# Kernel tuning notes

Measured on AMD Instinct MI355X. Metric: run time of the kernel, lower is better.

## Reference

```python
import jax, jax.numpy as jnp
import numpy as np

N, E, D_IN, L, H, U = 20000, 320000, 256, 4, 4, 64
HID = H * U  # 256
OUT = 64
LN_EPS = 1e-3  # keras LayerNormalization default epsilon
NEG_SLOPE = 0.2


def layer_norm(x, g, b):
    m = jnp.mean(x, axis=-1, keepdims=True)
    v = jnp.var(x, axis=-1, keepdims=True)
    return (x - m) * jax.lax.rsqrt(v + LN_EPS) * g + b


def gatv2(x, dst, src, Wl, Wr, a):
    # x: [N, HID]; Wl/Wr: [HID, H, U]; a: [H, U]
    zl = jnp.einsum('nd,dhu->nhu', x, Wl)  # target projection
    zr = jnp.einsum('nd,dhu->nhu', x, Wr)  # source projection / messages
    f = jax.nn.leaky_relu(zl[dst] + zr[src], NEG_SLOPE)       # [E, H, U]
    s = jnp.einsum('ehu,hu->eh', f, a)                        # [E, H]
    smax = jax.ops.segment_max(s, dst, num_segments=N)        # [N, H]
    es = jnp.exp(s - smax[dst])
    denom = jax.ops.segment_sum(es, dst, num_segments=N)      # [N, H]
    agg = jax.ops.segment_sum(es[:, :, None] * zr[src], dst, num_segments=N)
    agg = agg / (denom[:, :, None] + 1e-9)                    # [N, H, U]
    return agg.reshape(N, HID) + x  # residual (input dim == H*U)


def setup_inputs() -> dict:
    key = jax.random.key(0)
    ks = jax.random.split(key, 10)
    s_in = 1.0 / np.sqrt(D_IN)
    s_h = 1.0 / np.sqrt(HID)
    return {
        'x': jax.random.normal(ks[0], (N, D_IN), jnp.float32),
        'head_W': jax.random.normal(ks[1], (D_IN, HID), jnp.float32) * s_in,
        'head_b': jnp.zeros((HID,), jnp.float32),
        'ng_g': jnp.ones((L, HID), jnp.float32),
        'ng_b': jnp.zeros((L, HID), jnp.float32),
        'Wl': jax.random.normal(ks[2], (L, HID, H, U), jnp.float32) * s_h,
        'Wr': jax.random.normal(ks[3], (L, HID, H, U), jnp.float32) * s_h,
        'att': jax.random.normal(ks[4], (L, H, U), jnp.float32) * (1.0 / np.sqrt(U)),
        'nd_g': jnp.ones((L, HID), jnp.float32),
        'nd_b': jnp.zeros((L, HID), jnp.float32),
        'dense_W': jax.random.normal(ks[5], (L, HID, 4 * HID), jnp.float32) * s_h,
        'dense_b': jnp.zeros((L, 4 * HID), jnp.float32),
        'tail_W': jax.random.normal(ks[6], (HID, OUT), jnp.float32) * s_h,
        'tail_b': jnp.zeros((OUT,), jnp.float32),
        'edges': jax.random.randint(ks[7], (E, 2), 0, N, jnp.int32),
    }


def reference(x, head_W, head_b, ng_g, ng_b, Wl, Wr, att, nd_g, nd_b,
              dense_W, dense_b, tail_W, tail_b, edges):
    dst, src = edges[:, 0], edges[:, 1]
    h = x @ head_W + head_b  # head_layer
    for l in range(L):
        h = layer_norm(h, ng_g[l], ng_b[l])
        h = gatv2(h, dst, src, Wl[l], Wr[l], att[l])
        xr = layer_norm(h, nd_g[l], nd_b[l])
        # inference: dropout is identity
        d = jax.nn.gelu(xr @ dense_W[l] + dense_b[l], approximate=True)  # [N, 4*HID]
        h = d.reshape(N, 4, HID).sum(axis=1) + xr  # Add(split(.,4)) + residual
    return h @ tail_W + tail_b
```

## Files before the change

kernel.cpp:

```cpp
#include <hip/hip_runtime.h>
#include <cstdint>

#define NN 20000
#define EE 320000
#define DHID 256

typedef short bf16x8 __attribute__((ext_vector_type(8)));
typedef float f32x4 __attribute__((ext_vector_type(4)));


__device__ __forceinline__ float b2f(unsigned short u) {
    union { unsigned int i; float f; } v;
    v.i = ((unsigned int)u) << 16;
    return v.f;
}

__device__ __forceinline__ void b2f2(unsigned int w, float& lo, float& hi) {
    union { unsigned int i; float f; } a, c;
    a.i = w << 16;
    c.i = w & 0xffff0000u;
    lo = a.f;
    hi = c.f;
}

__device__ __forceinline__ unsigned short f2b(float x) {
    union { float f; unsigned int i; } v;
    v.f = x;
    unsigned int r = (v.i + 0x7FFFu + ((v.i >> 16) & 1u)) >> 16;
    return (unsigned short)r;
}

__device__ __forceinline__ float wave_sum(float v) {
#pragma unroll
    for (int m = 1; m < 64; m <<= 1) v += __shfl_xor(v, m);
    return v;
}

#define DPP_ROR_ADD(v, n)                                                                  \
    v += __int_as_float(__builtin_amdgcn_update_dpp(__float_as_int(v), __float_as_int(v),  \
                                                    0x120 + (n), 0xF, 0xF, 0))
__device__ __forceinline__ float quad16_sum(float v) {
    DPP_ROR_ADD(v, 8);
    DPP_ROR_ADD(v, 4);
    DPP_ROR_ADD(v, 2);
    DPP_ROR_ADD(v, 1);
    return v;
}

__device__ __forceinline__ float gelu_f(float x) {
    float x2 = x * x;
    float p  = fmaf(0.044715f, x2, 1.0f);
    float e  = __expf(x * p * 1.5957691216f);
    float r  = 1.0f / (e + 1.0f);
    return x - x * r;
}

__device__ __forceinline__ void gld16(const unsigned short* g, unsigned short* lds) {
    __builtin_amdgcn_global_load_lds((const __attribute__((address_space(1))) unsigned int*)g,
                                     (__attribute__((address_space(3))) unsigned int*)lds, 16, 0, 0);
}


__global__ void hist_kernel(const int* __restrict__ edges, int* __restrict__ counts, int E_) {
    int e = blockIdx.x * 256 + threadIdx.x;
    if (e >= E_) return;
    atomicAdd(&counts[edges[e * 2]], 1);
}

__global__ void pad_counts(const int* __restrict__ counts, int* __restrict__ pc, int n) {
    int i = blockIdx.x * 256 + threadIdx.x;
    if (i < n) pc[i] = (counts[i] + 3) & ~3;
}

__global__ __launch_bounds__(1024) void scan_block(const int* __restrict__ counts,
                                                   int* __restrict__ excl,
                                                   int* __restrict__ bsums, int n) {
    __shared__ int sd[1024];
    int tid = threadIdx.x;
    int i = blockIdx.x * 1024 + tid;
    int c = (i < n) ? counts[i] : 0;
    sd[tid] = c;
    __syncthreads();
#pragma unroll
    for (int off = 1; off < 1024; off <<= 1) {
        int v = (tid >= off) ? sd[tid - off] : 0;
        __syncthreads();
        sd[tid] += v;
        __syncthreads();
    }
    if (i < n) excl[i] = sd[tid] - c;
    if (tid == 1023) bsums[blockIdx.x] = sd[1023];
}

__global__ void scan_tops(int* __restrict__ bsums, int nb) {
    if (threadIdx.x == 0 && blockIdx.x == 0) {
        int run = 0;
        for (int i = 0; i < nb; ++i) { int t = bsums[i]; bsums[i] = run; run += t; }
    }
}

__global__ void scan_fix2(const int* __restrict__ excl, const int* __restrict__ bsums,
                          const int* __restrict__ counts,
                          int* __restrict__ astart, int* __restrict__ aend,
                          int* __restrict__ cursor, int n) {
    int i = blockIdx.x * 256 + threadIdx.x;
    if (i < n) {
        int v = excl[i] + bsums[i >> 10];
        astart[i] = v;
        cursor[i] = v;
        aend[i]   = v + counts[i];
    }
}

__global__ void scatter2(const int* __restrict__ edges, int* __restrict__ cursor,
                         unsigned int* __restrict__ soff, int E_) {
    int e = blockIdx.x * 256 + threadIdx.x;
    if (e >= E_) return;
    int dstn = edges[e * 2];
    int src  = edges[e * 2 + 1];
    int pos = atomicAdd(&cursor[dstn], 1);
    soff[pos] = (unsigned int)src << 10;
}


__global__ __launch_bounds__(256) void transpose_bf16(const float* __restrict__ W,
                                                      unsigned short* __restrict__ Wt,
                                                      int K, int M, size_t lsW, size_t lsT) {
    W  += (size_t)blockIdx.z * lsW;
    Wt += (size_t)blockIdx.z * lsT;
    __shared__ float sm[32][33];
    int m0 = blockIdx.x * 32, k0 = blockIdx.y * 32;
    int tx = threadIdx.x & 31, ty = threadIdx.x >> 5;
#pragma unroll
    for (int i = 0; i < 4; ++i)
        sm[ty + i * 8][tx] = W[(size_t)(k0 + ty + i * 8) * M + m0 + tx];
    __syncthreads();
#pragma unroll
    for (int i = 0; i < 4; ++i)
        Wt[(size_t)(m0 + ty + i * 8) * K + k0 + tx] = f2b(sm[tx][ty + i * 8]);
}

__global__ __launch_bounds__(256) void transpose_perm(const float* __restrict__ W,
                                                      unsigned short* __restrict__ Wt,
                                                      int K, int M, size_t lsW, size_t lsT) {
    W  += (size_t)blockIdx.z * lsW;
    Wt += (size_t)blockIdx.z * lsT;
    __shared__ float sm[32][33];
    int m0 = blockIdx.x * 32, k0 = blockIdx.y * 32;
    int tx = threadIdx.x & 31, ty = threadIdx.x >> 5;
#pragma unroll
    for (int i = 0; i < 4; ++i)
        sm[ty + i * 8][tx] = W[(size_t)(k0 + ty + i * 8) * M + m0 + tx];
    __syncthreads();
#pragma unroll
    for (int i = 0; i < 4; ++i) {
        int mm = m0 + ty + i * 8;
        int c = mm >> 8, j = mm & 255;
        int by = j >> 5, t = j & 31;
        int cc = (by << 7) | ((t >> 4) << 6) | (c << 4) | (t & 15);
        Wt[(size_t)cc * K + k0 + tx] = f2b(sm[tx][ty + i * 8]);
    }
}

__global__ void convert_bf16(const float* __restrict__ in, unsigned short* __restrict__ out, int n4) {
    int i = blockIdx.x * 256 + threadIdx.x;
    if (i >= n4) return;
    float4 v = *(const float4*)(in + (size_t)i * 4);
    ushort4 o;
    o.x = f2b(v.x); o.y = f2b(v.y); o.z = f2b(v.z); o.w = f2b(v.w);
    *(ushort4*)(out + (size_t)i * 4) = o;
}


__global__ __launch_bounds__(256) void ln_kernel(const float* __restrict__ X,
                                                 const float* __restrict__ g,
                                                 const float* __restrict__ b,
                                                 unsigned short* __restrict__ Yb, int nrows) {
    int row = blockIdx.x * 4 + (threadIdx.x >> 6);
    int lane = threadIdx.x & 63;
    if (row >= nrows) return;
    float4 v = *(const float4*)(X + (size_t)row * DHID + lane * 4);
    float sum = wave_sum(v.x + v.y + v.z + v.w);
    float sq  = wave_sum(v.x * v.x + v.y * v.y + v.z * v.z + v.w * v.w);
    float mean = sum * (1.0f / DHID);
    float var  = sq * (1.0f / DHID) - mean * mean;
    float r = rsqrtf(fmaxf(var, 0.0f) + 1e-3f);
    float4 gv = *(const float4*)(g + lane * 4);
    float4 bv = *(const float4*)(b + lane * 4);
    float4 o;
    o.x = (v.x - mean) * r * gv.x + bv.x;
    o.y = (v.y - mean) * r * gv.y + bv.y;
    o.z = (v.z - mean) * r * gv.z + bv.z;
    o.w = (v.w - mean) * r * gv.w + bv.w;
    ushort4 ob;
    ob.x = f2b(o.x); ob.y = f2b(o.y); ob.z = f2b(o.z); ob.w = f2b(o.w);
    *(ushort4*)(Yb + (size_t)row * DHID + lane * 4) = ob;
}

__global__ __launch_bounds__(256) void ln_dense(const unsigned short* __restrict__ d,
                                                const unsigned short* __restrict__ xrb,
                                                const float* __restrict__ g,
                                                const float* __restrict__ b,
                                                unsigned short* __restrict__ Yb, int nrows) {
    int row = blockIdx.x * 4 + (threadIdx.x >> 6);
    int lane = threadIdx.x & 63;
    if (row >= nrows) return;
    ushort4 xu = *(const ushort4*)(xrb + (size_t)row * DHID + lane * 4);
    ushort4 du = *(const ushort4*)(d   + (size_t)row * DHID + lane * 4);
    float4 v;
    v.x = b2f(xu.x) + b2f(du.x);
    v.y = b2f(xu.y) + b2f(du.y);
    v.z = b2f(xu.z) + b2f(du.z);
    v.w = b2f(xu.w) + b2f(du.w);
    float sum = wave_sum(v.x + v.y + v.z + v.w);
    float sq  = wave_sum(v.x * v.x + v.y * v.y + v.z * v.z + v.w * v.w);
    float mean = sum * (1.0f / DHID);
    float var  = sq * (1.0f / DHID) - mean * mean;
    float r = rsqrtf(fmaxf(var, 0.0f) + 1e-3f);
    float4 gv = *(const float4*)(g + lane * 4);
    float4 bv = *(const float4*)(b + lane * 4);
    float4 o;
    o.x = (v.x - mean) * r * gv.x + bv.x;
    o.y = (v.y - mean) * r * gv.y + bv.y;
    o.z = (v.z - mean) * r * gv.z + bv.z;
    o.w = (v.w - mean) * r * gv.w + bv.w;
    ushort4 ob;
    ob.x = f2b(o.x); ob.y = f2b(o.y); ob.z = f2b(o.z); ob.w = f2b(o.w);
    *(ushort4*)(Yb + (size_t)row * DHID + lane * 4) = ob;
}

__global__ __launch_bounds__(256) void combine_final(const unsigned short* __restrict__ d,
                                                     const unsigned short* __restrict__ xrb,
                                                     unsigned short* __restrict__ hb, int nrows) {
    int row = blockIdx.x * 4 + (threadIdx.x >> 6);
    int lane = threadIdx.x & 63;
    if (row >= nrows) return;
    ushort4 xu = *(const ushort4*)(xrb + (size_t)row * DHID + lane * 4);
    ushort4 du = *(const ushort4*)(d   + (size_t)row * DHID + lane * 4);
    ushort4 ob;
    ob.x = f2b(b2f(xu.x) + b2f(du.x));
    ob.y = f2b(b2f(xu.y) + b2f(du.y));
    ob.z = f2b(b2f(xu.z) + b2f(du.z));
    ob.w = f2b(b2f(xu.w) + b2f(du.w));
    *(ushort4*)(hb + (size_t)row * DHID + lane * 4) = ob;
}


#define CS_STRIDE 140
#define CS2_STRIDE 40

template <int EP>
__global__ __launch_bounds__(256, 3) void gemm128(const unsigned short* __restrict__ A,
                                                  const unsigned short* __restrict__ B,
                                                  const float* __restrict__ bias,
                                                  void* __restrict__ Cv, int nrows, int ncols) {
    __shared__ unsigned short smem[128 * CS_STRIDE];
    unsigned short* As = smem;
    unsigned short* Bs = smem + 8192;
    unsigned short* Cs = smem;
    const int bm = blockIdx.x * 128, bn = blockIdx.y * 128;
    if (bm >= nrows) return;
    const int tid  = threadIdx.x;
    const int w    = tid >> 6, lane = tid & 63;
    const int quad = lane >> 4, l16 = lane & 15;
    const int wm = w >> 1, wn = w & 1;

    const int srow = lane & 15;
    const int sg   = lane >> 4;
    int ga0 = min(bm + w * 32 + srow,      nrows - 1);
    int ga1 = min(bm + w * 32 + 16 + srow, nrows - 1);
    int gb0 = min(bn + w * 32 + srow,      ncols - 1);
    int gb1 = min(bn + w * 32 + 16 + srow, ncols - 1);
    const unsigned short* Ap0 = A + (size_t)ga0 * 256 + sg * 8;
    const unsigned short* Ap1 = A + (size_t)ga1 * 256 + sg * 8;
    const unsigned short* Bp0 = B + (size_t)gb0 * 256 + sg * 8;
    const unsigned short* Bp1 = B + (size_t)gb1 * 256 + sg * 8;
    unsigned short* la0 = As + (2 * w) * 1024;
    unsigned short* la1 = As + (2 * w + 1) * 1024;
    unsigned short* lb0 = Bs + (2 * w) * 1024;
    unsigned short* lb1 = Bs + (2 * w + 1) * 1024;

    f32x4 acc[4][4] = {};
    for (int k0 = 0; k0 < 256; k0 += 64) {
        gld16(Ap0 + k0,      la0);
        gld16(Ap0 + k0 + 32, la0 + 512);
        gld16(Ap1 + k0,      la1);
        gld16(Ap1 + k0 + 32, la1 + 512);
        gld16(Bp0 + k0,      lb0);
        gld16(Bp0 + k0 + 32, lb0 + 512);
        gld16(Bp1 + k0,      lb1);
        gld16(Bp1 + k0 + 32, lb1 + 512);
        __syncthreads();
#pragma unroll
        for (int kk = 0; kk < 2; ++kk) {
            bf16x8 a[4], b[4];
#pragma unroll
            for (int mi = 0; mi < 4; ++mi)
                a[mi] = *(const bf16x8*)(As + (wm * 4 + mi) * 1024 + (kk * 4 + quad) * 128 + l16 * 8);
#pragma unroll
            for (int ni = 0; ni < 4; ++ni)
                b[ni] = *(const bf16x8*)(Bs + (wn * 4 + ni) * 1024 + (kk * 4 + quad) * 128 + l16 * 8);
#pragma unroll
            for (int mi = 0; mi < 4; ++mi)
#pragma unroll
                for (int ni = 0; ni < 4; ++ni)
                    acc[mi][ni] = __builtin_amdgcn_mfma_f32_16x16x32_bf16(a[mi], b[ni], acc[mi][ni], 0, 0, 0);
        }
        __syncthreads();
    }

    if (EP == 0) {
#pragma unroll
        for (int ni = 0; ni < 4; ++ni) {
            int col = bn + wn * 64 + ni * 16 + l16;
            if (col >= ncols) continue;
            float bv = bias ? bias[col] : 0.0f;
#pragma unroll
            for (int mi = 0; mi < 4; ++mi) {
#pragma unroll
                for (int r = 0; r < 4; ++r) {
                    int row = bm + wm * 64 + mi * 16 + quad * 4 + r;
                    if (row < nrows) ((float*)Cv)[(size_t)row * ncols + col] = acc[mi][ni][r] + bv;
                }
            }
        }
    } else if (EP == 1) {
#pragma unroll
        for (int ni = 0; ni < 4; ++ni) {
            int lc = wn * 64 + ni * 16 + l16;
#pragma unroll
            for (int mi = 0; mi < 4; ++mi) {
#pragma unroll
                for (int r = 0; r < 4; ++r) {
                    int lr = wm * 64 + mi * 16 + quad * 4 + r;
                    Cs[lr * CS_STRIDE + lc] = f2b(acc[mi][ni][r]);
                }
            }
        }
        __syncthreads();
#pragma unroll
        for (int i = 0; i < 8; ++i) {
            int id = tid + 256 * i;
            int lr = id >> 4;
            int lc = (id & 15) * 8;
            int grow = bm + lr;
            if (grow < nrows) {
                uint4 val = *(const uint4*)(Cs + lr * CS_STRIDE + lc);
                *(uint4*)((unsigned short*)Cv + (size_t)grow * ncols + bn + lc) = val;
            }
        }
    } else {
        unsigned short* Cs2 = smem;
        int jfl = wn * 16 + l16;
        int jf  = (bn >> 2) + jfl;
        float bv0 = bias[jf];
        float bv1 = bias[256 + jf];
        float bv2 = bias[512 + jf];
        float bv3 = bias[768 + jf];
#pragma unroll
        for (int mi = 0; mi < 4; ++mi) {
#pragma unroll
            for (int r = 0; r < 4; ++r) {
                float v = gelu_f(acc[mi][0][r] + bv0) + gelu_f(acc[mi][1][r] + bv1)
                        + gelu_f(acc[mi][2][r] + bv2) + gelu_f(acc[mi][3][r] + bv3);
                int lr = wm * 64 + mi * 16 + quad * 4 + r;
                Cs2[lr * CS2_STRIDE + jfl] = f2b(v);
            }
        }
        __syncthreads();
#pragma unroll
        for (int i = 0; i < 2; ++i) {
            int id = tid + 256 * i;
            int lr = id >> 2;
            int q  = id & 3;
            int grow = bm + lr;
            if (grow < nrows) {
                uint4 val = *(const uint4*)(Cs2 + lr * CS2_STRIDE + q * 8);
                *(uint4*)((unsigned short*)Cv + (size_t)grow * 256 + (bn >> 2) + q * 8) = val;
            }
        }
    }
}


__global__ __launch_bounds__(64) void gat_fused(const unsigned short* __restrict__ zb,
                                                const float* __restrict__ att,
                                                const unsigned int* __restrict__ soff,
                                                const int* __restrict__ astart,
                                                const int* __restrict__ aend,
                                                const unsigned short* __restrict__ hnb,
                                                const float* __restrict__ g,
                                                const float* __restrict__ b,
                                                unsigned short* __restrict__ xrb, int nrows) {
    int lane = threadIdx.x;
    int n = blockIdx.x;
    int p0  = astart[n];
    int end = aend[n];

    ushort4 zlu = *(const ushort4*)(zb + (size_t)n * 512 + lane * 4);
    float zl0 = b2f(zlu.x), zl1 = b2f(zlu.y), zl2 = b2f(zlu.z), zl3 = b2f(zlu.w);
    float4 a4 = *(const float4*)(att + lane * 4);

    const char* zrb = (const char*)zb + 512;
    const unsigned int loff = (unsigned int)lane * 8u;

    float denom = 0.f;
    float ax = 0.f, ay = 0.f, az = 0.f, aw = 0.f;

    auto edge4 = [&](uint2 u0, uint2 u1, uint2 u2, uint2 u3, int pb) {
        float z00, z01, z02, z03, z10, z11, z12, z13;
        float z20, z21, z22, z23, z30, z31, z32, z33;
        b2f2(u0.x, z00, z01); b2f2(u0.y, z02, z03);
        b2f2(u1.x, z10, z11); b2f2(u1.y, z12, z13);
        b2f2(u2.x, z20, z21); b2f2(u2.y, z22, z23);
        b2f2(u3.x, z30, z31); b2f2(u3.y, z32, z33);

        float v00 = zl0 + z00, v01 = zl1 + z01, v02 = zl2 + z02, v03 = zl3 + z03;
        float v10 = zl0 + z10, v11 = zl1 + z11, v12 = zl2 + z12, v13 = zl3 + z13;
        float v20 = zl0 + z20, v21 = zl1 + z21, v22 = zl2 + z22, v23 = zl3 + z23;
        float v30 = zl0 + z30, v31 = zl1 + z31, v32 = zl2 + z32, v33 = zl3 + z33;
        v00 = fmaxf(v00, 0.2f * v00); v01 = fmaxf(v01, 0.2f * v01);
        v02 = fmaxf(v02, 0.2f * v02); v03 = fmaxf(v03, 0.2f * v03);
        v10 = fmaxf(v10, 0.2f * v10); v11 = fmaxf(v11, 0.2f * v11);
        v12 = fmaxf(v12, 0.2f * v12); v13 = fmaxf(v13, 0.2f * v13);
        v20 = fmaxf(v20, 0.2f * v20); v21 = fmaxf(v21, 0.2f * v21);
        v22 = fmaxf(v22, 0.2f * v22); v23 = fmaxf(v23, 0.2f * v23);
        v30 = fmaxf(v30, 0.2f * v30); v31 = fmaxf(v31, 0.2f * v31);
        v32 = fmaxf(v32, 0.2f * v32); v33 = fmaxf(v33, 0.2f * v33);
        float q0 = a4.x * v00 + a4.y * v01 + a4.z * v02 + a4.w * v03;
        float q1 = a4.x * v10 + a4.y * v11 + a4.z * v12 + a4.w * v13;
        float q2 = a4.x * v20 + a4.y * v21 + a4.z * v22 + a4.w * v23;
        float q3 = a4.x * v30 + a4.y * v31 + a4.z * v32 + a4.w * v33;
        float s0 = quad16_sum(q0);
        float s1 = quad16_sum(q1);
        float s2 = quad16_sum(q2);
        float s3 = quad16_sum(q3);
        float w0 = __expf(s0);
        float w1 = (pb + 1 < end) ? __expf(s1) : 0.0f;
        float w2 = (pb + 2 < end) ? __expf(s2) : 0.0f;
        float w3 = (pb + 3 < end) ? __expf(s3) : 0.0f;
        denom += (w0 + w1) + (w2 + w3);
        ax += (w0 * z00 + w1 * z10) + (w2 * z20 + w3 * z30);
        ay += (w0 * z01 + w1 * z11) + (w2 * z21 + w3 * z31);
        az += (w0 * z02 + w1 * z12) + (w2 * z22 + w3 * z32);
        aw += (w0 * z03 + w1 * z13) + (w2 * z23 + w3 * z33);
    };

    uint4 oA = *(const uint4*)(soff + p0);
    uint2 cA0 = *(const uint2*)(zrb + (oA.x + loff));
    uint2 cA1 = *(const uint2*)(zrb + (oA.y + loff));
    uint2 cA2 = *(const uint2*)(zrb + (oA.z + loff));
    uint2 cA3 = *(const uint2*)(zrb + (oA.w + loff));
    uint4 oB = *(const uint4*)(soff + p0 + 4);
    uint2 cB0 = *(const uint2*)(zrb + (oB.x + loff));
    uint2 cB1 = *(const uint2*)(zrb + (oB.y + loff));
    uint2 cB2 = *(const uint2*)(zrb + (oB.z + loff));
    uint2 cB3 = *(const uint2*)(zrb + (oB.w + loff));

    for (int p = p0; p < end; p += 8) {
        edge4(cA0, cA1, cA2, cA3, p);
        oA = *(const uint4*)(soff + p + 8);
        cA0 = *(const uint2*)(zrb + (oA.x + loff));
        cA1 = *(const uint2*)(zrb + (oA.y + loff));
        cA2 = *(const uint2*)(zrb + (oA.z + loff));
        cA3 = *(const uint2*)(zrb + (oA.w + loff));
        if (p + 4 >= end) break;
        edge4(cB0, cB1, cB2, cB3, p + 4);
        oB = *(const uint4*)(soff + p + 12);
        cB0 = *(const uint2*)(zrb + (oB.x + loff));
        cB1 = *(const uint2*)(zrb + (oB.y + loff));
        cB2 = *(const uint2*)(zrb + (oB.z + loff));
        cB3 = *(const uint2*)(zrb + (oB.w + loff));
    }

    size_t idx = (size_t)n * DHID + lane * 4;
    ushort4 ru = *(const ushort4*)(hnb + idx);
    float inv = 1.0f / (denom + 1e-9f);
    float4 o;
    o.x = ax * inv + b2f(ru.x);
    o.y = ay * inv + b2f(ru.y);
    o.z = az * inv + b2f(ru.z);
    o.w = aw * inv + b2f(ru.w);
    float sum = wave_sum(o.x + o.y + o.z + o.w);
    float sq  = wave_sum(o.x * o.x + o.y * o.y + o.z * o.z + o.w * o.w);
    float mean = sum * (1.0f / DHID);
    float var  = sq * (1.0f / DHID) - mean * mean;
    float rnorm = rsqrtf(fmaxf(var, 0.0f) + 1e-3f);
    float4 gv = *(const float4*)(g + lane * 4);
    float4 bv = *(const float4*)(b + lane * 4);
    float4 y;
    y.x = (o.x - mean) * rnorm * gv.x + bv.x;
    y.y = (o.y - mean) * rnorm * gv.y + bv.y;
    y.z = (o.z - mean) * rnorm * gv.z + bv.z;
    y.w = (o.w - mean) * rnorm * gv.w + bv.w;
    ushort4 ob;
    ob.x = f2b(y.x); ob.y = f2b(y.y); ob.z = f2b(y.z); ob.w = f2b(y.w);
    *(ushort4*)(xrb + idx) = ob;
}


extern "C" void kernel_launch(void* const* d_in, const int* in_sizes, int n_in,
                              void* d_out, int out_size, void* d_ws, size_t ws_size,
                              hipStream_t stream) {
    const float* x       = (const float*)d_in[0];
    const float* head_W  = (const float*)d_in[1];
    const float* head_b  = (const float*)d_in[2];
    const float* ng_g    = (const float*)d_in[3];
    const float* ng_b    = (const float*)d_in[4];
    const float* Wl      = (const float*)d_in[5];
    const float* Wr      = (const float*)d_in[6];
    const float* att     = (const float*)d_in[7];
    const float* nd_g    = (const float*)d_in[8];
    const float* nd_b    = (const float*)d_in[9];
    const float* dense_W = (const float*)d_in[10];
    const float* dense_b = (const float*)d_in[11];
    const float* tail_W  = (const float*)d_in[12];
    const float* tail_b  = (const float*)d_in[13];
    const int*   edges   = (const int*)d_in[14];
    float* out = (float*)d_out;

    const size_t NH = (size_t)NN * DHID;
    const int SOFF_LEN = EE + 4 * NN + 16;
    float* xr = (float*)d_ws;
    float* hn = xr + NH;
    unsigned short* hnb = (unsigned short*)(hn + NH);
    unsigned short* xrb = hnb + NH;
    unsigned short* U   = xrb + NH;
    unsigned short* zb  = U;
    unsigned short* d_buf = U;
    unsigned short* headT  = U + 4 * NH;
    unsigned short* WzT    = headT + 65536;
    unsigned short* denseT = WzT + 524288;
    unsigned short* tailT  = denseT + 1048576;
    int* counts  = (int*)(tailT + 16384);
    int* pcounts = counts + NN;
    int* bsums   = pcounts + NN;
    int* excl    = bsums + 32;
    int* cursor  = excl + NN;
    unsigned int* soff = (unsigned int*)hn;
    int* astart = (int*)(soff + SOFF_LEN);
    int* aendp  = astart + NN;

    hipMemsetAsync(counts, 0, NN * sizeof(int), stream);
    hipMemsetAsync(soff, 0, SOFF_LEN * sizeof(int), stream);
    hist_kernel<<<(EE + 255) / 256, 256, 0, stream>>>(edges, counts, EE);
    pad_counts<<<(NN + 255) / 256, 256, 0, stream>>>(counts, pcounts, NN);
    scan_block<<<(NN + 1023) / 1024, 1024, 0, stream>>>(pcounts, excl, bsums, NN);
    scan_tops<<<1, 64, 0, stream>>>(bsums, (NN + 1023) / 1024);
    scan_fix2<<<(NN + 255) / 256, 256, 0, stream>>>(excl, bsums, counts, astart, aendp, cursor, NN);
    scatter2<<<(EE + 255) / 256, 256, 0, stream>>>(edges, cursor, soff, EE);

    transpose_bf16<<<dim3(8, 8, 1), 256, 0, stream>>>(head_W, headT, 256, 256, 0, 0);
    transpose_bf16<<<dim3(8, 8, 4), 256, 0, stream>>>(Wl, WzT, 256, 256, 65536, 131072);
    transpose_bf16<<<dim3(8, 8, 4), 256, 0, stream>>>(Wr, WzT + 65536, 256, 256, 65536, 131072);
    transpose_perm<<<dim3(32, 8, 4), 256, 0, stream>>>(dense_W, denseT, 256, 1024, 262144, 262144);
    transpose_bf16<<<dim3(2, 8, 1), 256, 0, stream>>>(tail_W, tailT, 256, 64, 0, 0);
    convert_bf16<<<(int)(NH / 4 + 255) / 256, 256, 0, stream>>>(x, hnb, (int)(NH / 4));

    const int GXP = 160;
    gemm128<0><<<dim3(GXP, 2), 256, 0, stream>>>(hnb, headT, head_b, xr, NN, 256);

    for (int l = 0; l < 4; ++l) {
        if (l == 0)
            ln_kernel<<<NN / 4, 256, 0, stream>>>(xr, ng_g, ng_b, hnb, NN);
        else
            ln_dense<<<NN / 4, 256, 0, stream>>>(d_buf, xrb, ng_g + l * 256, ng_b + l * 256, hnb, NN);
        gemm128<1><<<dim3(GXP, 4), 256, 0, stream>>>(hnb, WzT + (size_t)l * 131072, nullptr, zb, NN, 512);
        gat_fused<<<NN, 64, 0, stream>>>(zb, att + l * 256, soff, astart, aendp, hnb,
                                         nd_g + l * 256, nd_b + l * 256, xrb, NN);
        gemm128<3><<<dim3(GXP, 8), 256, 0, stream>>>(xrb, denseT + (size_t)l * 262144,
                                                     dense_b + l * 1024, d_buf, NN, 1024);
    }
    combine_final<<<NN / 4, 256, 0, stream>>>(d_buf, xrb, hnb, NN);
    gemm128<0><<<dim3(GXP, 1), 256, 0, stream>>>(hnb, tailT, tail_b, out, NN, 64);
}
```

Before: 532.4 us.

## Deepen edge gather prefetch to four groups and fold scan launches

The aggregation loop now keeps four groups of four source-row gathers in flight instead of two, stepping by sixteen edges, and the padded offset buffer grows to cover the deeper lookahead. Separately, the padding of per-node counts is folded into the block scan, and the single-thread scan over block sums is replaced by each thread summing preceding block totals inside the fixup kernel. This removes two small launches and aims to hide more gather latency, at the cost of extra registers per lane, which may lower occupancy.

```diff
diff --git a/kernel.cpp b/kernel.cpp
--- a/kernel.cpp
+++ b/kernel.cpp
@@ -67,18 +67,13 @@
     atomicAdd(&counts[edges[e * 2]], 1);
 }
 
-__global__ void pad_counts(const int* __restrict__ counts, int* __restrict__ pc, int n) {
-    int i = blockIdx.x * 256 + threadIdx.x;
-    if (i < n) pc[i] = (counts[i] + 3) & ~3;
-}
-
 __global__ __launch_bounds__(1024) void scan_block(const int* __restrict__ counts,
                                                    int* __restrict__ excl,
                                                    int* __restrict__ bsums, int n) {
     __shared__ int sd[1024];
     int tid = threadIdx.x;
     int i = blockIdx.x * 1024 + tid;
-    int c = (i < n) ? counts[i] : 0;
+    int c = (i < n) ? ((counts[i] + 3) & ~3) : 0;
     sd[tid] = c;
     __syncthreads();
 #pragma unroll
@@ -90,13 +85,6 @@
     }
     if (i < n) excl[i] = sd[tid] - c;
     if (tid == 1023) bsums[blockIdx.x] = sd[1023];
-}
-
-__global__ void scan_tops(int* __restrict__ bsums, int nb) {
-    if (threadIdx.x == 0 && blockIdx.x == 0) {
-        int run = 0;
-        for (int i = 0; i < nb; ++i) { int t = bsums[i]; bsums[i] = run; run += t; }
-    }
 }
 
 __global__ void scan_fix2(const int* __restrict__ excl, const int* __restrict__ bsums,
@@ -105,7 +93,10 @@
                           int* __restrict__ cursor, int n) {
     int i = blockIdx.x * 256 + threadIdx.x;
     if (i < n) {
-        int v = excl[i] + bsums[i >> 10];
+        int blk = i >> 10;
+        int base = 0;
+        for (int j = 0; j < blk; ++j) base += bsums[j];
+        int v = excl[i] + base;
         astart[i] = v;
         cursor[i] = v;
         aend[i]   = v + counts[i];
@@ -456,21 +447,45 @@
     uint2 cB1 = *(const uint2*)(zrb + (oB.y + loff));
     uint2 cB2 = *(const uint2*)(zrb + (oB.z + loff));
     uint2 cB3 = *(const uint2*)(zrb + (oB.w + loff));
-
-    for (int p = p0; p < end; p += 8) {
+    uint4 oC = *(const uint4*)(soff + p0 + 8);
+    uint2 cC0 = *(const uint2*)(zrb + (oC.x + loff));
+    uint2 cC1 = *(const uint2*)(zrb + (oC.y + loff));
+    uint2 cC2 = *(const uint2*)(zrb + (oC.z + loff));
+    uint2 cC3 = *(const uint2*)(zrb + (oC.w + loff));
+    uint4 oD = *(const uint4*)(soff + p0 + 12);
+    uint2 cD0 = *(const uint2*)(zrb + (oD.x + loff));
+    uint2 cD1 = *(const uint2*)(zrb + (oD.y + loff));
+    uint2 cD2 = *(const uint2*)(zrb + (oD.z + loff));
+    uint2 cD3 = *(const uint2*)(zrb + (oD.w + loff));
+
+    for (int p = p0; p < end; p += 16) {
         edge4(cA0, cA1, cA2, cA3, p);
-        oA = *(const uint4*)(soff + p + 8);
+        oA = *(const uint4*)(soff + p + 16);
         cA0 = *(const uint2*)(zrb + (oA.x + loff));
         cA1 = *(const uint2*)(zrb + (oA.y + loff));
         cA2 = *(const uint2*)(zrb + (oA.z + loff));
         cA3 = *(const uint2*)(zrb + (oA.w + loff));
         if (p + 4 >= end) break;
         edge4(cB0, cB1, cB2, cB3, p + 4);
-        oB = *(const uint4*)(soff + p + 12);
+        oB = *(const uint4*)(soff + p + 20);
         cB0 = *(const uint2*)(zrb + (oB.x + loff));
         cB1 = *(const uint2*)(zrb + (oB.y + loff));
         cB2 = *(const uint2*)(zrb + (oB.z + loff));
         cB3 = *(const uint2*)(zrb + (oB.w + loff));
+        if (p + 8 >= end) break;
+        edge4(cC0, cC1, cC2, cC3, p + 8);
+        oC = *(const uint4*)(soff + p + 24);
+        cC0 = *(const uint2*)(zrb + (oC.x + loff));
+        cC1 = *(const uint2*)(zrb + (oC.y + loff));
+        cC2 = *(const uint2*)(zrb + (oC.z + loff));
+        cC3 = *(const uint2*)(zrb + (oC.w + loff));
+        if (p + 12 >= end) break;
+        edge4(cD0, cD1, cD2, cD3, p + 12);
+        oD = *(const uint4*)(soff + p + 28);
+        cD0 = *(const uint2*)(zrb + (oD.x + loff));
+        cD1 = *(const uint2*)(zrb + (oD.y + loff));
+        cD2 = *(const uint2*)(zrb + (oD.z + loff));
+        cD3 = *(const uint2*)(zrb + (oD.w + loff));
     }
 
     size_t idx = (size_t)n * DHID + lane * 4;
@@ -520,7 +535,7 @@
     float* out = (float*)d_out;
 
     const size_t NH = (size_t)NN * DHID;
-    const int SOFF_LEN = EE + 4 * NN + 16;
+    const int SOFF_LEN = EE + 4 * NN + 48;
     float* xr = (float*)d_ws;
     float* hn = xr + NH;
     unsigned short* hnb = (unsigned short*)(hn + NH);
@@ -533,8 +548,7 @@
     unsigned short* denseT = WzT + 524288;
     unsigned short* tailT  = denseT + 1048576;
     int* counts  = (int*)(tailT + 16384);
-    int* pcounts = counts + NN;
-    int* bsums   = pcounts + NN;
+    int* bsums   = counts + NN;
     int* excl    = bsums + 32;
     int* cursor  = excl + NN;
     unsigned int* soff = (unsigned int*)hn;
@@ -544,9 +558,7 @@
     hipMemsetAsync(counts, 0, NN * sizeof(int), stream);
     hipMemsetAsync(soff, 0, SOFF_LEN * sizeof(int), stream);
     hist_kernel<<<(EE + 255) / 256, 256, 0, stream>>>(edges, counts, EE);
-    pad_counts<<<(NN + 255) / 256, 256, 0, stream>>>(counts, pcounts, NN);
-    scan_block<<<(NN + 1023) / 1024, 1024, 0, stream>>>(pcounts, excl, bsums, NN);
-    scan_tops<<<1, 64, 0, stream>>>(bsums, (NN + 1023) / 1024);
+    scan_block<<<(NN + 1023) / 1024, 1024, 0, stream>>>(counts, excl, bsums, NN);
     scan_fix2<<<(NN + 255) / 256, 256, 0, stream>>>(excl, bsums, counts, astart, aendp, cursor, NN);
     scatter2<<<(EE + 255) / 256, 256, 0, stream>>>(edges, cursor, soff, EE);
 
```

After: 538.1 us. About the same (+1.1%).
